# Kernel tuning notes

Hardware: AMD Instinct MI355X
Metric: run time of the kernel (lower is better)

## Reference

```python
import jax, jax.numpy as jnp
import numpy as np
import math

B, I, O = 512, 512, 512
MEXHAT_NORM = 2.0 / (math.sqrt(3.0) * math.pi ** 0.25)
BN_EPS = 1e-5


def setup_inputs() -> dict:
    key = jax.random.key(0)
    kx, kw = jax.random.split(key, 2)
    x = jax.random.normal(kx, (B, I), dtype=jnp.float32)
    scale = jnp.ones((I, O), dtype=jnp.float32)
    bias = jnp.zeros((I, O), dtype=jnp.float32)
    # kaiming_uniform_ with a=sqrt(5): bound = sqrt(6 / ((1 + a^2) * fan_in)) = 1/sqrt(fan_in)
    bound = 1.0 / math.sqrt(I)
    weight = jax.random.uniform(kw, (I, O), dtype=jnp.float32, minval=-bound, maxval=bound)
    # BatchNorm1d affine params
    gamma = jnp.ones((O,), dtype=jnp.float32)
    beta = jnp.zeros((O,), dtype=jnp.float32)
    return {"x": x, "scale": scale, "bias": bias, "weight": weight,
            "gamma": gamma, "beta": beta}


def _mexhat_kan(x, scale, bias, weight):
    # x: (B, I); scale/bias/weight: (I, O)
    t = (x[:, :, None] - bias[None, :, :]) / scale[None, :, :]      # (B, I, O)
    t2 = t * t
    wav = MEXHAT_NORM * (t2 - 1.0) * jnp.exp(-0.5 * t2)             # Mexican hat
    return jnp.einsum('bio,io->bo', wav, weight)                    # reduce over in_features


def _batchnorm_train(y, gamma, beta):
    # BatchNorm1d in training mode: biased batch statistics over the batch dim
    mean = jnp.mean(y, axis=0)
    var = jnp.mean((y - mean) ** 2, axis=0)
    return (y - mean) * jax.lax.rsqrt(var + BN_EPS) * gamma + beta


def reference(x, scale, bias, weight, gamma, beta):
    y = _mexhat_kan(x, scale, bias, weight)   # (B, O)
    return _batchnorm_train(y, gamma, beta)
```

## Files before the change

### kernel.cpp

```cpp
#include <hip/hip_runtime.h>
#include <math.h>

#define B_ 512
#define I_ 512
#define O_ 512
#define BO_ (B_*O_)

#define ZV 16

#define TB 64
#define TO 16
#define KI 16
#define ZN 8
#define NIZ (I_/ZN)
#define NCHZ (NIZ/KI)
#define LXS (TB + 4)

#define SQH    0.84932180028801904f
#define MN_   (-1.2023679775792928f)
#define NN_   (-0.86732507058407750f)
#define BN_EPS (1e-5f)

#if defined(__has_builtin)
#if __has_builtin(__builtin_amdgcn_exp2f)
#define EXP2F(v) __builtin_amdgcn_exp2f(v)
#endif
#endif
#ifndef EXP2F
#define EXP2F(v) exp2f(v)
#endif

__global__ __launch_bounds__(256) void kanV(
    const float* __restrict__ x, const float* __restrict__ scale,
    const float* __restrict__ bias, const float* __restrict__ weight,
    float* __restrict__ pY)
{
    __shared__ float4 Lp[16][4][16];
    __shared__ float  Lx[16][128];

    const int fid = blockIdx.x;
    const int ot  = fid & 7;
    const int bt  = (fid >> 3) & 3;
    const int iz  = fid >> 5;

    const int o0 = ot * 64;
    const int b0 = bt * 128;
    const int z0 = iz * 32;

    const int t   = threadIdx.x;
    const int oq  = t & 15;
    const int bq  = t >> 4;
    const int si  = t >> 4;
    const int so4 = t & 15;
    const int lb  = t >> 1;
    const int lh  = t & 1;

    float4 a[8];
    #pragma unroll
    for (int r = 0; r < 8; ++r) a[r] = make_float4(0.f, 0.f, 0.f, 0.f);

    for (int ch = 0; ch < 2; ++ch) {
        const int i0 = z0 + ch * 16;

        const size_t g = (size_t)(i0 + si) * O_ + o0 + so4 * 4;
        const float4 s4 = *reinterpret_cast<const float4*>(&scale[g]);
        const float4 b4 = *reinterpret_cast<const float4*>(&bias[g]);
        const float4 w4 = *reinterpret_cast<const float4*>(&weight[g]);
        const size_t xg = (size_t)(b0 + lb) * I_ + i0 + lh * 8;
        const float4 xv0 = *reinterpret_cast<const float4*>(&x[xg]);
        const float4 xv1 = *reinterpret_cast<const float4*>(&x[xg + 4]);

        __syncthreads();

        {
            const float c = SQH * __builtin_amdgcn_rcpf(s4.x);
            Lp[si][0][so4] = make_float4(c, -b4.x * c, MN_ * w4.x, NN_ * w4.x);
        }
        {
            const float c = SQH * __builtin_amdgcn_rcpf(s4.y);
            Lp[si][1][so4] = make_float4(c, -b4.y * c, MN_ * w4.y, NN_ * w4.y);
        }
        {
            const float c = SQH * __builtin_amdgcn_rcpf(s4.z);
            Lp[si][2][so4] = make_float4(c, -b4.z * c, MN_ * w4.z, NN_ * w4.z);
        }
        {
            const float c = SQH * __builtin_amdgcn_rcpf(s4.w);
            Lp[si][3][so4] = make_float4(c, -b4.w * c, MN_ * w4.w, NN_ * w4.w);
        }
        Lx[lh * 8 + 0][lb] = xv0.x;
        Lx[lh * 8 + 1][lb] = xv0.y;
        Lx[lh * 8 + 2][lb] = xv0.z;
        Lx[lh * 8 + 3][lb] = xv0.w;
        Lx[lh * 8 + 4][lb] = xv1.x;
        Lx[lh * 8 + 5][lb] = xv1.y;
        Lx[lh * 8 + 6][lb] = xv1.z;
        Lx[lh * 8 + 7][lb] = xv1.w;

        __syncthreads();

#define EVQ(xs, A)                                                           \
    {                                                                        \
        { const float h  = fmaf((xs), p0.x, p0.y);                           \
          const float un = -h * h;                                           \
          const float e  = EXP2F(un);                                        \
          const float gg = fmaf(un, p0.z, p0.w);                             \
          A.x = fmaf(gg, e, A.x); }                                          \
        { const float h  = fmaf((xs), p1.x, p1.y);                           \
          const float un = -h * h;                                           \
          const float e  = EXP2F(un);                                        \
          const float gg = fmaf(un, p1.z, p1.w);                             \
          A.y = fmaf(gg, e, A.y); }                                          \
        { const float h  = fmaf((xs), p2.x, p2.y);                           \
          const float un = -h * h;                                           \
          const float e  = EXP2F(un);                                        \
          const float gg = fmaf(un, p2.z, p2.w);                             \
          A.z = fmaf(gg, e, A.z); }                                          \
        { const float h  = fmaf((xs), p3.x, p3.y);                           \
          const float un = -h * h;                                           \
          const float e  = EXP2F(un);                                        \
          const float gg = fmaf(un, p3.z, p3.w);                             \
          A.w = fmaf(gg, e, A.w); }                                          \
    }

        #pragma unroll 2
        for (int ii = 0; ii < 16; ++ii) {
            const float4 p0 = Lp[ii][0][oq];
            const float4 p1 = Lp[ii][1][oq];
            const float4 p2 = Lp[ii][2][oq];
            const float4 p3 = Lp[ii][3][oq];
            const float4 xA = *reinterpret_cast<const float4*>(&Lx[ii][bq * 8 + 0]);
            const float4 xB = *reinterpret_cast<const float4*>(&Lx[ii][bq * 8 + 4]);
            EVQ(xA.x, a[0]);
            EVQ(xA.y, a[1]);
            EVQ(xA.z, a[2]);
            EVQ(xA.w, a[3]);
            EVQ(xB.x, a[4]);
            EVQ(xB.y, a[5]);
            EVQ(xB.z, a[6]);
            EVQ(xB.w, a[7]);
        }
#undef EVQ
    }

    #pragma unroll
    for (int r = 0; r < 8; ++r) {
        const size_t base = ((size_t)iz * B_ + b0 + bq * 8 + r) * O_ + o0 + oq * 4;
        *reinterpret_cast<float4*>(&pY[base]) = a[r];
    }
}

__global__ __launch_bounds__(256) void kanZ(
    const float* __restrict__ x, const float* __restrict__ scale,
    const float* __restrict__ bias, const float* __restrict__ weight,
    float* __restrict__ pY)
{
    __shared__ float Lx[KI][LXS];
    __shared__ float Lp[KI][TO][4];

    const int fid = blockIdx.x;
    const int xcd = fid & 7;
    const int seq = fid >> 3;
    const int ot  = xcd * 4 + (seq & 3);
    const int by  = (seq >> 2) & 7;
    const int iz  = seq >> 5;

    const int o0 = ot * TO;
    const int b0 = by * TB;
    const int z0 = iz * NIZ;

    const int t   = threadIdx.x;
    const int to  = t & (TO - 1);
    const int tb4 = t >> 4;
    const int lb  = t >> 2;
    const int lq  = t & 3;
    const int li  = t >> 4;
    const int lo  = t & 15;

    float acc0 = 0.f, acc1 = 0.f, acc2 = 0.f, acc3 = 0.f;

    for (int ch = 0; ch < NCHZ; ++ch) {
        const int i0 = z0 + ch * KI;
        const float4 xv = *reinterpret_cast<const float4*>(
            &x[(size_t)(b0 + lb) * I_ + i0 + lq * 4]);
        const int pidx = (i0 + li) * O_ + o0 + lo;
        const float sc = scale[pidx];
        const float bi = bias[pidx];
        const float w  = weight[pidx];

        __syncthreads();
        Lx[lq * 4 + 0][lb] = xv.x;
        Lx[lq * 4 + 1][lb] = xv.y;
        Lx[lq * 4 + 2][lb] = xv.z;
        Lx[lq * 4 + 3][lb] = xv.w;
        const float c = SQH * __builtin_amdgcn_rcpf(sc);
        Lp[li][lo][0] = c;
        Lp[li][lo][1] = -bi * c;
        Lp[li][lo][2] = MN_ * w;
        Lp[li][lo][3] = NN_ * w;
        __syncthreads();

        #pragma unroll
        for (int ii = 0; ii < KI; ++ii) {
            const float4 p  = *reinterpret_cast<const float4*>(&Lp[ii][to][0]);
            const float4 x4 = *reinterpret_cast<const float4*>(&Lx[ii][tb4 * 4]);
            {
                const float h  = fmaf(x4.x, p.x, p.y);
                const float un = -h * h;
                const float e  = EXP2F(un);
                const float gg = fmaf(un, p.z, p.w);
                acc0 = fmaf(gg, e, acc0);
            }
            {
                const float h  = fmaf(x4.y, p.x, p.y);
                const float un = -h * h;
                const float e  = EXP2F(un);
                const float gg = fmaf(un, p.z, p.w);
                acc1 = fmaf(gg, e, acc1);
            }
            {
                const float h  = fmaf(x4.z, p.x, p.y);
                const float un = -h * h;
                const float e  = EXP2F(un);
                const float gg = fmaf(un, p.z, p.w);
                acc2 = fmaf(gg, e, acc2);
            }
            {
                const float h  = fmaf(x4.w, p.x, p.y);
                const float un = -h * h;
                const float e  = EXP2F(un);
                const float gg = fmaf(un, p.z, p.w);
                acc3 = fmaf(gg, e, acc3);
            }
        }
    }

    const size_t base = ((size_t)iz * B_ + b0 + tb4 * 4) * O_ + o0 + to;
    pY[base + 0 * O_] = acc0;
    pY[base + 1 * O_] = acc1;
    pY[base + 2 * O_] = acc2;
    pY[base + 3 * O_] = acc3;
}

template <int NZ>
__global__ __launch_bounds__(256) void comb_bn(
    const float* __restrict__ pY,
    const float* __restrict__ gamma, const float* __restrict__ beta,
    float* __restrict__ y)
{
    __shared__ float Ws[4][8];
    __shared__ float Ac[8];

    const int bid = blockIdx.x;
    const int o4  = (bid & 7) * 64 + (bid >> 3) * 4;
    const int t   = threadIdx.x;

    float4 v[2];
    float sx = 0.f, sy = 0.f, sz = 0.f, sw = 0.f;
    float qx = 0.f, qy = 0.f, qz = 0.f, qw = 0.f;
    #pragma unroll
    for (int r = 0; r < 2; ++r) {
        const int b = t + 256 * r;
        const size_t base = (size_t)b * O_ + o4;
        float4 a = *reinterpret_cast<const float4*>(&pY[base]);
        #pragma unroll
        for (int z = 1; z < NZ; ++z) {
            const float4 p = *reinterpret_cast<const float4*>(&pY[(size_t)z * BO_ + base]);
            a.x += p.x; a.y += p.y; a.z += p.z; a.w += p.w;
        }
        v[r] = a;
        sx += a.x; sy += a.y; sz += a.z; sw += a.w;
        qx += a.x * a.x; qy += a.y * a.y; qz += a.z * a.z; qw += a.w * a.w;
    }

    #pragma unroll
    for (int m = 1; m < 64; m <<= 1) {
        sx += __shfl_xor(sx, m); sy += __shfl_xor(sy, m);
        sz += __shfl_xor(sz, m); sw += __shfl_xor(sw, m);
        qx += __shfl_xor(qx, m); qy += __shfl_xor(qy, m);
        qz += __shfl_xor(qz, m); qw += __shfl_xor(qw, m);
    }
    if ((t & 63) == 0) {
        const int wv = t >> 6;
        Ws[wv][0] = sx; Ws[wv][1] = sy; Ws[wv][2] = sz; Ws[wv][3] = sw;
        Ws[wv][4] = qx; Ws[wv][5] = qy; Ws[wv][6] = qz; Ws[wv][7] = qw;
    }
    __syncthreads();
    if (t < 4) {
        const float s  = Ws[0][t]     + Ws[1][t]     + Ws[2][t]     + Ws[3][t];
        const float q  = Ws[0][t + 4] + Ws[1][t + 4] + Ws[2][t + 4] + Ws[3][t + 4];
        const float mean = s * (1.0f / B_);
        const float var  = q * (1.0f / B_) - mean * mean;
        const float inv  = rsqrtf(var + BN_EPS);
        const float a = gamma[o4 + t] * inv;
        Ac[t]     = a;
        Ac[t + 4] = fmaf(-mean, a, beta[o4 + t]);
    }
    __syncthreads();

    const float4 a4 = *reinterpret_cast<const float4*>(&Ac[0]);
    const float4 c4 = *reinterpret_cast<const float4*>(&Ac[4]);
    #pragma unroll
    for (int r = 0; r < 2; ++r) {
        const int b = t + 256 * r;
        float4 o;
        o.x = fmaf(v[r].x, a4.x, c4.x);
        o.y = fmaf(v[r].y, a4.y, c4.y);
        o.z = fmaf(v[r].z, a4.z, c4.z);
        o.w = fmaf(v[r].w, a4.w, c4.w);
        *reinterpret_cast<float4*>(&y[(size_t)b * O_ + o4]) = o;
    }
}


extern "C" void kernel_launch(void* const* d_in, const int* in_sizes, int n_in,
                              void* d_out, int out_size, void* d_ws, size_t ws_size,
                              hipStream_t stream) {
    const float* x      = (const float*)d_in[0];
    const float* scale  = (const float*)d_in[1];
    const float* bias   = (const float*)d_in[2];
    const float* weight = (const float*)d_in[3];
    const float* gamma  = (const float*)d_in[4];
    const float* beta   = (const float*)d_in[5];
    float* out = (float*)d_out;

    const size_t pYV_b = (size_t)ZV * BO_ * sizeof(float);
    const size_t pYZ_b = (size_t)ZN * BO_ * sizeof(float);

    if (ws_size >= pYV_b) {
        float* pY = (float*)d_ws;
        kanV<<<8 * 4 * ZV, 256, 0, stream>>>(x, scale, bias, weight, pY);
        comb_bn<ZV><<<O_ / 4, 256, 0, stream>>>(pY, gamma, beta, out);
    } else if (ws_size >= pYZ_b) {
        float* pY = (float*)d_ws;
        kanZ<<<32 * 8 * 8, 256, 0, stream>>>(x, scale, bias, weight, pY);
        comb_bn<ZN><<<O_ / 4, 256, 0, stream>>>(pY, gamma, beta, out);
    }
}
```

Baseline: 34.50 us.

## Halve output tile per block, split loaders by role, add XCD-aware block mapping

The main compute kernel now handles a 32-wide output tile instead of 64, which doubles the grid to 1024 blocks, and each thread keeps 16 accumulators instead of 32. Block indices are remapped so that neighbouring output tiles land on the same XCD. Parameter loads and x loads are split between the two halves of the block rather than done by every thread. The aim is higher occupancy and less register pressure. In exchange, each x element staged in shared memory is reused across fewer outputs, and the output writes become float2 instead of float4.

```diff
diff --git a/kernel.cpp b/kernel.cpp
--- a/kernel.cpp
+++ b/kernel.cpp
@@ -6,7 +6,7 @@
 #define O_ 512
 #define BO_ (B_*O_)
 
-#define ZV 16
+#define ZU 16
 
 #define TB 64
 #define TO 16
@@ -30,123 +30,132 @@
 #define EXP2F(v) exp2f(v)
 #endif
 
-__global__ __launch_bounds__(256) void kanV(
+__global__ __launch_bounds__(256) void kanU(
     const float* __restrict__ x, const float* __restrict__ scale,
     const float* __restrict__ bias, const float* __restrict__ weight,
     float* __restrict__ pY)
 {
-    __shared__ float4 Lp[16][4][16];
+    __shared__ float4 Lp[16][2][16];
     __shared__ float  Lx[16][128];
 
     const int fid = blockIdx.x;
-    const int ot  = fid & 7;
-    const int bt  = (fid >> 3) & 3;
-    const int iz  = fid >> 5;
-
-    const int o0 = ot * 64;
+    const int xcd = fid & 7;
+    const int seq = fid >> 3;
+    const int otl = seq & 1;
+    const int bt  = (seq >> 1) & 3;
+    const int iz  = seq >> 3;
+
+    const int o0 = (xcd * 2 + otl) * 32;
     const int b0 = bt * 128;
     const int z0 = iz * 32;
 
-    const int t   = threadIdx.x;
-    const int oq  = t & 15;
-    const int bq  = t >> 4;
-    const int si  = t >> 4;
-    const int so4 = t & 15;
-    const int lb  = t >> 1;
-    const int lh  = t & 1;
-
-    float4 a[8];
-    #pragma unroll
-    for (int r = 0; r < 8; ++r) a[r] = make_float4(0.f, 0.f, 0.f, 0.f);
+    const int t  = threadIdx.x;
+    const int oq = t & 15;
+    const int bq = t >> 4;
+
+    const int isP = (t < 128);
+    const int pi  = t >> 3;
+    const int pq  = t & 7;
+    const int tx  = t - 128;
+
+    float4 aA0 = {0,0,0,0}, aB0 = {0,0,0,0};
+    float4 aA1 = {0,0,0,0}, aB1 = {0,0,0,0};
 
     for (int ch = 0; ch < 2; ++ch) {
         const int i0 = z0 + ch * 16;
 
-        const size_t g = (size_t)(i0 + si) * O_ + o0 + so4 * 4;
-        const float4 s4 = *reinterpret_cast<const float4*>(&scale[g]);
-        const float4 b4 = *reinterpret_cast<const float4*>(&bias[g]);
-        const float4 w4 = *reinterpret_cast<const float4*>(&weight[g]);
-        const size_t xg = (size_t)(b0 + lb) * I_ + i0 + lh * 8;
-        const float4 xv0 = *reinterpret_cast<const float4*>(&x[xg]);
-        const float4 xv1 = *reinterpret_cast<const float4*>(&x[xg + 4]);
+        float4 s4, b4, w4, xv0, xv1, xv2, xv3;
+        if (isP) {
+            const size_t g = (size_t)(i0 + pi) * O_ + o0 + pq * 4;
+            s4 = *reinterpret_cast<const float4*>(&scale[g]);
+            b4 = *reinterpret_cast<const float4*>(&bias[g]);
+            w4 = *reinterpret_cast<const float4*>(&weight[g]);
+        } else {
+            const size_t xg = (size_t)(b0 + tx) * I_ + i0;
+            xv0 = *reinterpret_cast<const float4*>(&x[xg + 0]);
+            xv1 = *reinterpret_cast<const float4*>(&x[xg + 4]);
+            xv2 = *reinterpret_cast<const float4*>(&x[xg + 8]);
+            xv3 = *reinterpret_cast<const float4*>(&x[xg + 12]);
+        }
 
         __syncthreads();
 
-        {
-            const float c = SQH * __builtin_amdgcn_rcpf(s4.x);
-            Lp[si][0][so4] = make_float4(c, -b4.x * c, MN_ * w4.x, NN_ * w4.x);
-        }
-        {
-            const float c = SQH * __builtin_amdgcn_rcpf(s4.y);
-            Lp[si][1][so4] = make_float4(c, -b4.y * c, MN_ * w4.y, NN_ * w4.y);
-        }
-        {
-            const float c = SQH * __builtin_amdgcn_rcpf(s4.z);
-            Lp[si][2][so4] = make_float4(c, -b4.z * c, MN_ * w4.z, NN_ * w4.z);
-        }
-        {
-            const float c = SQH * __builtin_amdgcn_rcpf(s4.w);
-            Lp[si][3][so4] = make_float4(c, -b4.w * c, MN_ * w4.w, NN_ * w4.w);
-        }
-        Lx[lh * 8 + 0][lb] = xv0.x;
-        Lx[lh * 8 + 1][lb] = xv0.y;
-        Lx[lh * 8 + 2][lb] = xv0.z;
-        Lx[lh * 8 + 3][lb] = xv0.w;
-        Lx[lh * 8 + 4][lb] = xv1.x;
-        Lx[lh * 8 + 5][lb] = xv1.y;
-        Lx[lh * 8 + 6][lb] = xv1.z;
-        Lx[lh * 8 + 7][lb] = xv1.w;
+        if (isP) {
+            {
+                const float c = SQH * __builtin_amdgcn_rcpf(s4.x);
+                const int ol = pq * 4 + 0;
+                Lp[pi][ol & 1][ol >> 1] = make_float4(c, -b4.x * c, MN_ * w4.x, NN_ * w4.x);
+            }
+            {
+                const float c = SQH * __builtin_amdgcn_rcpf(s4.y);
+                const int ol = pq * 4 + 1;
+                Lp[pi][ol & 1][ol >> 1] = make_float4(c, -b4.y * c, MN_ * w4.y, NN_ * w4.y);
+            }
+            {
+                const float c = SQH * __builtin_amdgcn_rcpf(s4.z);
+                const int ol = pq * 4 + 2;
+                Lp[pi][ol & 1][ol >> 1] = make_float4(c, -b4.z * c, MN_ * w4.z, NN_ * w4.z);
+            }
+            {
+                const float c = SQH * __builtin_amdgcn_rcpf(s4.w);
+                const int ol = pq * 4 + 3;
+                Lp[pi][ol & 1][ol >> 1] = make_float4(c, -b4.w * c, MN_ * w4.w, NN_ * w4.w);
+            }
+        } else {
+            Lx[ 0][tx] = xv0.x;  Lx[ 1][tx] = xv0.y;
+            Lx[ 2][tx] = xv0.z;  Lx[ 3][tx] = xv0.w;
+            Lx[ 4][tx] = xv1.x;  Lx[ 5][tx] = xv1.y;
+            Lx[ 6][tx] = xv1.z;  Lx[ 7][tx] = xv1.w;
+            Lx[ 8][tx] = xv2.x;  Lx[ 9][tx] = xv2.y;
+            Lx[10][tx] = xv2.z;  Lx[11][tx] = xv2.w;
+            Lx[12][tx] = xv3.x;  Lx[13][tx] = xv3.y;
+            Lx[14][tx] = xv3.z;  Lx[15][tx] = xv3.w;
+        }
 
         __syncthreads();
 
-#define EVQ(xs, A)                                                           \
+#define EV2(xs, A0, A1)                                                      \
     {                                                                        \
         { const float h  = fmaf((xs), p0.x, p0.y);                           \
           const float un = -h * h;                                           \
           const float e  = EXP2F(un);                                        \
           const float gg = fmaf(un, p0.z, p0.w);                             \
-          A.x = fmaf(gg, e, A.x); }                                          \
+          (A0) = fmaf(gg, e, (A0)); }                                        \
         { const float h  = fmaf((xs), p1.x, p1.y);                           \
           const float un = -h * h;                                           \
           const float e  = EXP2F(un);                                        \
           const float gg = fmaf(un, p1.z, p1.w);                             \
-          A.y = fmaf(gg, e, A.y); }                                          \
-        { const float h  = fmaf((xs), p2.x, p2.y);                           \
-          const float un = -h * h;                                           \
-          const float e  = EXP2F(un);                                        \
-          const float gg = fmaf(un, p2.z, p2.w);                             \
-          A.z = fmaf(gg, e, A.z); }                                          \
-        { const float h  = fmaf((xs), p3.x, p3.y);                           \
-          const float un = -h * h;                                           \
-          const float e  = EXP2F(un);                                        \
-          const float gg = fmaf(un, p3.z, p3.w);                             \
-          A.w = fmaf(gg, e, A.w); }                                          \
-    }
-
-        #pragma unroll 2
+          (A1) = fmaf(gg, e, (A1)); }                                        \
+    }
+
+        #pragma unroll 4
         for (int ii = 0; ii < 16; ++ii) {
             const float4 p0 = Lp[ii][0][oq];
             const float4 p1 = Lp[ii][1][oq];
-            const float4 p2 = Lp[ii][2][oq];
-            const float4 p3 = Lp[ii][3][oq];
             const float4 xA = *reinterpret_cast<const float4*>(&Lx[ii][bq * 8 + 0]);
             const float4 xB = *reinterpret_cast<const float4*>(&Lx[ii][bq * 8 + 4]);
-            EVQ(xA.x, a[0]);
-            EVQ(xA.y, a[1]);
-            EVQ(xA.z, a[2]);
-            EVQ(xA.w, a[3]);
-            EVQ(xB.x, a[4]);
-            EVQ(xB.y, a[5]);
-            EVQ(xB.z, a[6]);
-            EVQ(xB.w, a[7]);
-        }
-#undef EVQ
-    }
-
-    #pragma unroll
-    for (int r = 0; r < 8; ++r) {
-        const size_t base = ((size_t)iz * B_ + b0 + bq * 8 + r) * O_ + o0 + oq * 4;
-        *reinterpret_cast<float4*>(&pY[base]) = a[r];
+            EV2(xA.x, aA0.x, aA1.x);
+            EV2(xA.y, aA0.y, aA1.y);
+            EV2(xA.z, aA0.z, aA1.z);
+            EV2(xA.w, aA0.w, aA1.w);
+            EV2(xB.x, aB0.x, aB1.x);
+            EV2(xB.y, aB0.y, aB1.y);
+            EV2(xB.z, aB0.z, aB1.z);
+            EV2(xB.w, aB0.w, aB1.w);
+        }
+#undef EV2
+    }
+
+    {
+        const size_t rb = ((size_t)iz * B_ + b0 + bq * 8) * O_ + o0 + oq * 2;
+        *reinterpret_cast<float2*>(&pY[rb + 0 * O_]) = make_float2(aA0.x, aA1.x);
+        *reinterpret_cast<float2*>(&pY[rb + 1 * O_]) = make_float2(aA0.y, aA1.y);
+        *reinterpret_cast<float2*>(&pY[rb + 2 * O_]) = make_float2(aA0.z, aA1.z);
+        *reinterpret_cast<float2*>(&pY[rb + 3 * O_]) = make_float2(aA0.w, aA1.w);
+        *reinterpret_cast<float2*>(&pY[rb + 4 * O_]) = make_float2(aB0.x, aB1.x);
+        *reinterpret_cast<float2*>(&pY[rb + 5 * O_]) = make_float2(aB0.y, aB1.y);
+        *reinterpret_cast<float2*>(&pY[rb + 6 * O_]) = make_float2(aB0.z, aB1.z);
+        *reinterpret_cast<float2*>(&pY[rb + 7 * O_]) = make_float2(aB0.w, aB1.w);
     }
 }
 
@@ -324,13 +333,13 @@
     const float* beta   = (const float*)d_in[5];
     float* out = (float*)d_out;
 
-    const size_t pYV_b = (size_t)ZV * BO_ * sizeof(float);
+    const size_t pYU_b = (size_t)ZU * BO_ * sizeof(float);
     const size_t pYZ_b = (size_t)ZN * BO_ * sizeof(float);
 
-    if (ws_size >= pYV_b) {
+    if (ws_size >= pYU_b) {
         float* pY = (float*)d_ws;
-        kanV<<<8 * 4 * ZV, 256, 0, stream>>>(x, scale, bias, weight, pY);
-        comb_bn<ZV><<<O_ / 4, 256, 0, stream>>>(pY, gamma, beta, out);
+        kanU<<<8 * 2 * 4 * ZU, 256, 0, stream>>>(x, scale, bias, weight, pY);
+        comb_bn<ZU><<<O_ / 4, 256, 0, stream>>>(pY, gamma, beta, out);
     } else if (ws_size >= pYZ_b) {
         float* pY = (float*)d_ws;
         kanZ<<<32 * 8 * 8, 256, 0, stream>>>(x, scale, bias, weight, pY);
```

Result: no change. 35.14 us (+1.9%).
